# Optimization experiments

Measured on AMD Instinct MI355X. Metric: run time of the kernel, lower is better.

The kernel has to match this reference:

```python
import jax, jax.numpy as jnp
import numpy as np

DIM = 2048
NHEAD = 16
HEAD_DIM = DIM // NHEAD
FF_HIDDEN = 5632
EPS = 1e-6


def setup_inputs() -> dict:
    key = jax.random.key(0)
    ks = jax.random.split(key, 8)
    B, S = 2, 2048
    sd = 0.02
    return {
        "x": jax.random.normal(ks[0], (B, S, DIM), dtype=jnp.float32),
        "w_qkv": jax.random.normal(ks[1], (DIM, 3 * DIM), dtype=jnp.float32) * sd,
        "w_out": jax.random.normal(ks[2], (DIM, DIM), dtype=jnp.float32) * sd,
        "g1": jnp.ones((DIM,), dtype=jnp.float32),
        "g2": jnp.ones((DIM,), dtype=jnp.float32),
        "w1": jax.random.normal(ks[3], (DIM, FF_HIDDEN), dtype=jnp.float32) * sd,
        "w3": jax.random.normal(ks[4], (DIM, FF_HIDDEN), dtype=jnp.float32) * sd,
        "w2": jax.random.normal(ks[5], (FF_HIDDEN, DIM), dtype=jnp.float32) * sd,
    }


def _rmsnorm(x, g):
    rms = jnp.sqrt(jnp.mean(x * x, axis=-1, keepdims=True) + EPS)
    return x / rms * g


def _attention(x, w_qkv, w_out):
    B, S, D = x.shape
    qkv = x @ w_qkv  # [B,S,3D]
    q, k, v = jnp.split(qkv, 3, axis=-1)
    # [B,H,S,hd]
    q = q.reshape(B, S, NHEAD, HEAD_DIM).transpose(0, 2, 1, 3)
    k = k.reshape(B, S, NHEAD, HEAD_DIM).transpose(0, 2, 1, 3)
    v = v.reshape(B, S, NHEAD, HEAD_DIM).transpose(0, 2, 1, 3)
    scores = jnp.einsum("bhqd,bhkd->bhqk", q, k) / jnp.sqrt(jnp.float32(HEAD_DIM))
    causal = jnp.tril(jnp.ones((S, S), dtype=bool))
    scores = jnp.where(causal, scores, -jnp.inf)
    attn = jax.nn.softmax(scores, axis=-1)
    out = jnp.einsum("bhqk,bhkd->bhqd", attn, v)
    out = out.transpose(0, 2, 1, 3).reshape(B, S, D)
    return out @ w_out


def _swiglu(x, w1, w3, w2):
    return (jax.nn.silu(x @ w1) * (x @ w3)) @ w2


def reference(x, w_qkv, w_out, g1, g2, w1, w3, w2):
    x = x + _attention(_rmsnorm(x, g1), w_qkv, w_out)
    x = x + _swiglu(_rmsnorm(x, g2), w1, w3, w2)
    return x
```

## Files before the change

### kernel.cpp

```cpp
#include <hip/hip_runtime.h>
#include <hip/hip_bf16.h>
#include <stdint.h>


typedef __attribute__((ext_vector_type(8))) short bf16x8;
typedef __attribute__((ext_vector_type(8))) unsigned short u16x8;
typedef __attribute__((ext_vector_type(4))) float f32x4;

__device__ __forceinline__ unsigned short f2bf(float f) {
  union { float f; unsigned int u; } c; c.f = f;
  unsigned int u = c.u + 0x7fffu + ((c.u >> 16) & 1u);
  return (unsigned short)(u >> 16);
}
__device__ __forceinline__ float bf2f(unsigned short h) {
  union { unsigned int u; float f; } c; c.u = ((unsigned int)h) << 16;
  return c.f;
}

__device__ __forceinline__ void gload16(const void* g, void* l) {
  __builtin_amdgcn_global_load_lds(
      (const __attribute__((address_space(1))) void*)g,
      (__attribute__((address_space(3))) void*)l, 16, 0, 0);
}

__global__ __launch_bounds__(256)
void rmsnorm_bf16(const float* __restrict__ x, const float* __restrict__ g,
                  unsigned short* __restrict__ y)
{
  const long row = blockIdx.x;
  const float* xr = x + row * 2048;
  const int t = threadIdx.x;
  float4 a = *(const float4*)(xr + t * 8);
  float4 b = *(const float4*)(xr + t * 8 + 4);
  float ss = a.x*a.x + a.y*a.y + a.z*a.z + a.w*a.w
           + b.x*b.x + b.y*b.y + b.z*b.z + b.w*b.w;
#pragma unroll
  for (int off = 32; off >= 1; off >>= 1) ss += __shfl_xor(ss, off, 64);
  __shared__ float sm[4];
  if ((t & 63) == 0) sm[t >> 6] = ss;
  __syncthreads();
  float inv = rsqrtf((sm[0] + sm[1] + sm[2] + sm[3]) * (1.0f / 2048.0f) + 1e-6f);
  float4 ga = *(const float4*)(g + t * 8);
  float4 gb = *(const float4*)(g + t * 8 + 4);
  u16x8 ov;
  ov[0] = f2bf(a.x * inv * ga.x); ov[1] = f2bf(a.y * inv * ga.y);
  ov[2] = f2bf(a.z * inv * ga.z); ov[3] = f2bf(a.w * inv * ga.w);
  ov[4] = f2bf(b.x * inv * gb.x); ov[5] = f2bf(b.y * inv * gb.y);
  ov[6] = f2bf(b.z * inv * gb.z); ov[7] = f2bf(b.w * inv * gb.w);
  *(u16x8*)(y + row * 2048 + t * 8) = ov;
}

__global__ __launch_bounds__(256)
void transpose_w(const float* __restrict__ in, unsigned short* __restrict__ outp,
                 int K, int N)
{
  __shared__ float tile[32][33];
  const int c0 = blockIdx.x * 32, r0 = blockIdx.y * 32;
  const int cx = threadIdx.x & 31, ry = threadIdx.x >> 5;
#pragma unroll
  for (int i = 0; i < 4; i++)
    tile[ry + i * 8][cx] = in[(long)(r0 + ry + i * 8) * N + c0 + cx];
  __syncthreads();
#pragma unroll
  for (int i = 0; i < 4; i++)
    outp[(long)(c0 + ry + i * 8) * K + r0 + cx] = f2bf(tile[cx][ry + i * 8]);
}

template<int EPI>
__global__ __launch_bounds__(256)
void gemm_bt(const unsigned short* __restrict__ A,
             const unsigned short* __restrict__ Bt,
             void* __restrict__ Cout,
             const float* __restrict__ res,
             const unsigned short* __restrict__ mulsrc,
             unsigned short* __restrict__ vTout,
             int M, int N, int K)
{
  __shared__ unsigned short lds[2 * 128 * 64];
  const int tid = threadIdx.x;
  const int lane = tid & 63, wave = tid >> 6;
  const int wr = wave >> 1, wc = wave & 1;
  const int l15 = lane & 15, lg = lane >> 4;

  const int nwg = gridDim.x * gridDim.y;
  int wg = blockIdx.y * gridDim.x + blockIdx.x;
  wg = (wg & 7) * (nwg >> 3) + (wg >> 3);
  const int bx = wg % gridDim.x, by = wg / gridDim.x;
  const long m0 = (long)by * 128, n0 = (long)bx * 128;

  f32x4 acc[4][4];
#pragma unroll
  for (int m = 0; m < 4; m++)
#pragma unroll
    for (int n = 0; n < 4; n++) acc[m][n] = f32x4{0.f, 0.f, 0.f, 0.f};

  const int rsub = lane >> 3;
  const int csw = (lane & 7) ^ rsub;
  const unsigned short* Ab = A + (m0 + wave * 32 + rsub) * (long)K + csw * 8;
  const unsigned short* Bb = Bt + (n0 + wave * 32 + rsub) * (long)K + csw * 8;
  unsigned short* Al = lds + wave * 2048;
  unsigned short* Bl = lds + 8192 + wave * 2048;

  for (int kt = 0; kt < K; kt += 64) {
    __syncthreads();
#pragma unroll
    for (int i = 0; i < 4; i++) {
      gload16(Ab + (long)(i * 8) * K + kt, Al + i * 512);
      gload16(Bb + (long)(i * 8) * K + kt, Bl + i * 512);
    }
    __syncthreads();
#pragma unroll
    for (int kc = 0; kc < 2; kc++) {
      bf16x8 af[4], bfr[4];
#pragma unroll
      for (int m = 0; m < 4; m++) {
        int row = wr * 64 + m * 16 + l15;
        int off = row * 128 + ((kc * 64 + lg * 16) ^ ((row & 7) << 4));
        af[m] = *(const bf16x8*)((const char*)lds + off);
      }
#pragma unroll
      for (int n = 0; n < 4; n++) {
        int row = wc * 64 + n * 16 + l15;
        int off = 16384 + row * 128 + ((kc * 64 + lg * 16) ^ ((row & 7) << 4));
        bfr[n] = *(const bf16x8*)((const char*)lds + off);
      }
#pragma unroll
      for (int m = 0; m < 4; m++)
#pragma unroll
        for (int n = 0; n < 4; n++)
          acc[m][n] = __builtin_amdgcn_mfma_f32_16x16x32_bf16(af[m], bfr[n], acc[m][n], 0, 0, 0);
    }
  }

  if (EPI == 3) {
#pragma unroll
    for (int m = 0; m < 4; m++)
#pragma unroll
      for (int n = 0; n < 4; n++)
#pragma unroll
        for (int r = 0; r < 4; r++) {
          long row = m0 + wr * 64 + m * 16 + lg * 4 + r;
          long col = n0 + wc * 64 + n * 16 + l15;
          ((float*)Cout)[row * N + col] = acc[m][n][r] + res[row * N + col];
        }
    return;
  }

  __syncthreads();
  unsigned short* Cl = lds;
#pragma unroll
  for (int m = 0; m < 4; m++)
#pragma unroll
    for (int n = 0; n < 4; n++)
#pragma unroll
      for (int r = 0; r < 4; r++) {
        float v = acc[m][n][r];
        if (EPI == 1) v = v / (1.f + __expf(-v));
        int row = wr * 64 + m * 16 + lg * 4 + r;
        int col = wc * 64 + n * 16 + l15;
        Cl[row * 128 + (((col >> 3) ^ (row >> 3)) & 15) * 8 + (col & 7)] = f2bf(v);
      }
  __syncthreads();
#pragma unroll
  for (int r8 = 0; r8 < 8; r8++) {
    int id = tid + r8 * 256;
    int row = id >> 4, c = (id & 15) * 8;
    int ch = (id & 15) ^ (row >> 3);
    long grow = m0 + row, gcol = n0 + c;
    u16x8 v = *(const u16x8*)(Cl + row * 128 + ch * 8);
    if (EPI == 2) {
      u16x8 mm = *(const u16x8*)(mulsrc + grow * N + gcol);
#pragma unroll
      for (int j = 0; j < 8; j++) v[j] = f2bf(bf2f(v[j]) * bf2f(mm[j]));
    }
    *(u16x8*)((unsigned short*)Cout + grow * N + gcol) = v;
  }

  if (EPI == 0 && vTout != nullptr && n0 >= 4096) {
    const int hh = (int)((n0 - 4096) >> 7);
    const int b = (int)(m0 >> 11);
    const long s0 = m0 & 2047;
    unsigned short* vtb = vTout + ((long)(b * 16 + hh) * 128) * 2048;
#pragma unroll
    for (int r8 = 0; r8 < 8; r8++) {
      int id = tid + r8 * 256;
      int d = id >> 4, sc = (id & 15) * 8;
      int ch = ((d >> 3) ^ (id & 15)) & 15;
      u16x8 v;
#pragma unroll
      for (int j = 0; j < 8; j++) v[j] = Cl[(sc + j) * 128 + ch * 8 + (d & 7)];
      *(u16x8*)(vtb + (long)d * 2048 + s0 + sc) = v;
    }
  }
}

#define QSTEP(qf, mrow, lrow, o, qb, isdiag) do {                              \
    f32x4 sacc[4];                                                             \
    __builtin_amdgcn_s_setprio(1);                                             \
    _Pragma("unroll")                                                          \
    for (int cg = 0; cg < 4; cg++) {                                           \
      f32x4 a = f32x4{0.f, 0.f, 0.f, 0.f};                                     \
      _Pragma("unroll")                                                        \
      for (int kc = 0; kc < 4; kc++) {                                         \
        int krow = cg * 16 + l15;                                              \
        bf16x8 kf = *(const bf16x8*)((char*)Klds +                             \
            (krow * 256 + ((kc * 64 + lg * 16) ^ ((krow & 7) << 4))));         \
        a = __builtin_amdgcn_mfma_f32_16x16x32_bf16(qf[kc], kf, a, 0, 0, 0);   \
      }                                                                        \
      sacc[cg] = a;                                                            \
    }                                                                          \
    __builtin_amdgcn_s_setprio(0);                                             \
    float p[4][4], pm[4];                                                      \
    _Pragma("unroll")                                                          \
    for (int r = 0; r < 4; r++) pm[r] = -1e30f;                                \
    _Pragma("unroll")                                                          \
    for (int cg = 0; cg < 4; cg++)                                             \
      _Pragma("unroll")                                                        \
      for (int r = 0; r < 4; r++) {                                            \
        float v = sacc[cg][r] * scale;                                         \
        if (isdiag) {                                                          \
          int kvg = kv0 + cg * 16 + l15;                                       \
          int qg = qb + w * 16 + lg * 4 + r;                                   \
          if (kvg > qg) v = -1e30f;                                            \
        }                                                                      \
        p[cg][r] = v;                                                          \
        pm[r] = fmaxf(pm[r], v);                                               \
      }                                                                        \
    _Pragma("unroll")                                                          \
    for (int r = 0; r < 4; r++) {                                              \
      _Pragma("unroll")                                                        \
      for (int off = 1; off < 16; off <<= 1)                                   \
        pm[r] = fmaxf(pm[r], __shfl_xor(pm[r], off, 64));                      \
      float mn = fmaxf(mrow[r], pm[r]);                                        \
      float al = __expf(mrow[r] - mn);                                         \
      mrow[r] = mn;                                                            \
      float s = 0.f;                                                           \
      _Pragma("unroll")                                                        \
      for (int cg = 0; cg < 4; cg++) { p[cg][r] = __expf(p[cg][r] - mn); s += p[cg][r]; } \
      _Pragma("unroll")                                                        \
      for (int off = 1; off < 16; off <<= 1)                                   \
        s += __shfl_xor(s, off, 64);                                           \
      lrow[r] = lrow[r] * al + s;                                              \
      _Pragma("unroll")                                                        \
      for (int dg = 0; dg < 8; dg++) o[dg][r] *= al;                           \
    }                                                                          \
    _Pragma("unroll")                                                          \
    for (int cg = 0; cg < 4; cg++)                                             \
      _Pragma("unroll")                                                        \
      for (int r = 0; r < 4; r++) {                                            \
        int q = lg * 4 + r;                                                    \
        *((unsigned short*)((char*)&Plds[w][0] +                               \
            (q * 128 + (((cg * 16 + l15) * 2) ^ ((q & 7) << 4))))) = f2bf(p[cg][r]); \
      }                                                                        \
    asm volatile("s_waitcnt lgkmcnt(0)" ::: "memory");                         \
    __builtin_amdgcn_sched_barrier(0);                                         \
    __builtin_amdgcn_s_setprio(1);                                             \
    _Pragma("unroll")                                                          \
    for (int kc = 0; kc < 2; kc++) {                                           \
      bf16x8 pa = *(const bf16x8*)((char*)&Plds[w][0] +                        \
          (l15 * 128 + ((kc * 64 + lg * 16) ^ ((l15 & 7) << 4))));             \
      _Pragma("unroll")                                                        \
      for (int dg = 0; dg < 8; dg++) {                                         \
        int d = dg * 16 + l15;                                                 \
        bf16x8 vf = *(const bf16x8*)((char*)Vlds +                             \
            (d * 128 + ((kc * 64 + lg * 16) ^ ((d & 7) << 4))));               \
        o[dg] = __builtin_amdgcn_mfma_f32_16x16x32_bf16(pa, vf, o[dg], 0, 0, 0); \
      }                                                                        \
    }                                                                          \
    __builtin_amdgcn_s_setprio(0);                                             \
  } while (0)

__global__ __launch_bounds__(256, 2)
void attn_fwd(const unsigned short* __restrict__ qkv,
              const unsigned short* __restrict__ vT,
              unsigned short* __restrict__ out)
{
  __shared__ unsigned short Klds[64 * 128];
  __shared__ unsigned short Vlds[128 * 64];
  __shared__ unsigned short Plds[4][16 * 64];
  const int tid = threadIdx.x, lane = tid & 63, w = tid >> 6;
  const int l15 = lane & 15, lg = lane >> 4;

  const int nwg = gridDim.x * gridDim.y;
  int wg = blockIdx.y * gridDim.x + blockIdx.x;
  wg = (wg & 7) * (nwg >> 3) + (wg >> 3);
  const int ip = wg % 16;
  const int bh = wg / 16;
  const int b = bh >> 4, hh = bh & 15;

  const int qbA = ip * 64, qbB = (31 - ip) * 64;
  const long base = (long)b * 2048 * 6144;
  const int qoff = hh * 128, koff = 2048 + hh * 128;
  const unsigned short* vTg = vT + (long)bh * (128 * 2048);

  bf16x8 qfA[4], qfB[4];
  {
    long qrA = qbA + w * 16 + l15, qrB = qbB + w * 16 + l15;
#pragma unroll
    for (int kc = 0; kc < 4; kc++) {
      qfA[kc] = *(const bf16x8*)(qkv + base + qrA * 6144 + qoff + kc * 32 + lg * 8);
      qfB[kc] = *(const bf16x8*)(qkv + base + qrB * 6144 + qoff + kc * 32 + lg * 8);
    }
  }
  f32x4 oA[8], oB[8];
#pragma unroll
  for (int dg = 0; dg < 8; dg++) {
    oA[dg] = f32x4{0.f, 0.f, 0.f, 0.f};
    oB[dg] = f32x4{0.f, 0.f, 0.f, 0.f};
  }
  float mA[4] = {-1e30f, -1e30f, -1e30f, -1e30f}, lA[4] = {0.f, 0.f, 0.f, 0.f};
  float mB[4] = {-1e30f, -1e30f, -1e30f, -1e30f}, lB[4] = {0.f, 0.f, 0.f, 0.f};
  const float scale = 0.08838834764831845f;

  const int s_st = tid >> 4, d0 = (tid & 15) * 8;
  const int vrow = tid >> 3, vc = tid & 7;

  const int nt = 32 - ip;
  for (int t = 0; t < nt; t++) {
    const int kv0 = t * 64;
#pragma unroll
    for (int u = 0; u < 4; u++) {
      int srow = s_st + u * 16;
      uint4 kk = *(const uint4*)(qkv + base + (long)(kv0 + srow) * 6144 + koff + d0);
      *(uint4*)((char*)Klds + (srow * 256 + ((d0 * 2) ^ ((srow & 7) << 4)))) = kk;
    }
#pragma unroll
    for (int u = 0; u < 4; u++) {
      int d = vrow + u * 32;
      uint4 vv = *(const uint4*)(vTg + (long)d * 2048 + kv0 + vc * 8);
      *(uint4*)((char*)Vlds + (d * 128 + ((vc * 16) ^ ((d & 7) << 4)))) = vv;
    }
    __syncthreads();

    if (t <= ip) QSTEP(qfA, mA, lA, oA, qbA, (t == ip));
    QSTEP(qfB, mB, lB, oB, qbB, (t == nt - 1));

    __syncthreads();
  }

#pragma unroll
  for (int r = 0; r < 4; r++) {
    float invA = 1.f / lA[r], invB = 1.f / lB[r];
    long rowA = (long)b * 2048 + qbA + w * 16 + lg * 4 + r;
    long rowB = (long)b * 2048 + qbB + w * 16 + lg * 4 + r;
#pragma unroll
    for (int dg = 0; dg < 8; dg++) {
      out[rowA * 2048 + hh * 128 + dg * 16 + l15] = f2bf(oA[dg][r] * invA);
      out[rowB * 2048 + hh * 128 + dg * 16 + l15] = f2bf(oB[dg][r] * invB);
    }
  }
}

extern "C" void kernel_launch(void* const* d_in, const int* in_sizes, int n_in,
                              void* d_out, int out_size, void* d_ws, size_t ws_size,
                              hipStream_t stream)
{
  const float* x     = (const float*)d_in[0];
  const float* w_qkv = (const float*)d_in[1];
  const float* w_out = (const float*)d_in[2];
  const float* g1    = (const float*)d_in[3];
  const float* g2    = (const float*)d_in[4];
  const float* w1    = (const float*)d_in[5];
  const float* w3    = (const float*)d_in[6];
  const float* w2    = (const float*)d_in[7];
  float* outp = (float*)d_out;
  char* ws = (char*)d_ws;

  unsigned short* wT  = (unsigned short*)(ws);
  unsigned short* y   = (unsigned short*)(ws + 25165824);
  unsigned short* qkv = (unsigned short*)(ws + 41943040);
  unsigned short* att = (unsigned short*)(ws + 92274688);
  float*          x1  = (float*)(ws + 109051904);
  unsigned short* s1  = (unsigned short*)(ws + 142606336);
  unsigned short* vTb = s1;
  unsigned short* h   = qkv;

  rmsnorm_bf16<<<4096, 256, 0, stream>>>(x, g1, y);
  transpose_w<<<dim3(192, 64), 256, 0, stream>>>(w_qkv, wT, 2048, 6144);
  gemm_bt<0><<<dim3(48, 32), 256, 0, stream>>>(y, wT, qkv, nullptr, nullptr, vTb, 4096, 6144, 2048);
  attn_fwd<<<dim3(16, 32), 256, 0, stream>>>(qkv, vTb, att);
  transpose_w<<<dim3(64, 64), 256, 0, stream>>>(w_out, wT, 2048, 2048);
  gemm_bt<3><<<dim3(16, 32), 256, 0, stream>>>(att, wT, x1, x, nullptr, nullptr, 4096, 2048, 2048);

  rmsnorm_bf16<<<4096, 256, 0, stream>>>(x1, g2, y);
  transpose_w<<<dim3(176, 64), 256, 0, stream>>>(w1, wT, 2048, 5632);
  gemm_bt<1><<<dim3(44, 32), 256, 0, stream>>>(y, wT, s1, nullptr, nullptr, nullptr, 4096, 5632, 2048);
  transpose_w<<<dim3(176, 64), 256, 0, stream>>>(w3, wT, 2048, 5632);
  gemm_bt<2><<<dim3(44, 32), 256, 0, stream>>>(y, wT, h, nullptr, s1, nullptr, 4096, 5632, 2048);
  transpose_w<<<dim3(64, 176), 256, 0, stream>>>(w2, wT, 5632, 2048);
  gemm_bt<3><<<dim3(16, 32), 256, 0, stream>>>(h, wT, outp, x1, nullptr, nullptr, 4096, 2048, 5632);
}
```

Baseline: 711.0 us.

## Use 64-row GEMM tiles for N=2048 projections and store residual in bf16

Adds a gemm_mt64 kernel with 64x128 tiles for the two N=2048 GEMMs (out-projection and down-projection). This doubles the workgroup count from 512 to 1024 so more CUs have work. The intermediate residual x1 is now stored in bf16 rather than fp32, and a new bf16-input rmsnorm reads it. The final GEMM adds the bf16 residual back. The new kernel has a simpler single-buffered K loop, and the bf16 residual loses precision in the skip connection.

```diff
diff --git a/kernel.cpp b/kernel.cpp
--- a/kernel.cpp
+++ b/kernel.cpp
@@ -51,6 +51,34 @@
 }
 
 __global__ __launch_bounds__(256)
+void rmsnorm_bf16_in(const unsigned short* __restrict__ x, const float* __restrict__ g,
+                     unsigned short* __restrict__ y)
+{
+  const long row = blockIdx.x;
+  const unsigned short* xr = x + row * 2048;
+  const int t = threadIdx.x;
+  u16x8 iv = *(const u16x8*)(xr + t * 8);
+  float v[8];
+  float ss = 0.f;
+#pragma unroll
+  for (int j = 0; j < 8; j++) { v[j] = bf2f(iv[j]); ss += v[j] * v[j]; }
+#pragma unroll
+  for (int off = 32; off >= 1; off >>= 1) ss += __shfl_xor(ss, off, 64);
+  __shared__ float sm[4];
+  if ((t & 63) == 0) sm[t >> 6] = ss;
+  __syncthreads();
+  float inv = rsqrtf((sm[0] + sm[1] + sm[2] + sm[3]) * (1.0f / 2048.0f) + 1e-6f);
+  float4 ga = *(const float4*)(g + t * 8);
+  float4 gb = *(const float4*)(g + t * 8 + 4);
+  u16x8 ov;
+  ov[0] = f2bf(v[0] * inv * ga.x); ov[1] = f2bf(v[1] * inv * ga.y);
+  ov[2] = f2bf(v[2] * inv * ga.z); ov[3] = f2bf(v[3] * inv * ga.w);
+  ov[4] = f2bf(v[4] * inv * gb.x); ov[5] = f2bf(v[5] * inv * gb.y);
+  ov[6] = f2bf(v[6] * inv * gb.z); ov[7] = f2bf(v[7] * inv * gb.w);
+  *(u16x8*)(y + row * 2048 + t * 8) = ov;
+}
+
+__global__ __launch_bounds__(256)
 void transpose_w(const float* __restrict__ in, unsigned short* __restrict__ outp,
                  int K, int N)
 {
@@ -191,6 +219,110 @@
       for (int j = 0; j < 8; j++) v[j] = Cl[(sc + j) * 128 + ch * 8 + (d & 7)];
       *(u16x8*)(vtb + (long)d * 2048 + s0 + sc) = v;
     }
+  }
+}
+
+template<int EPI>
+__global__ __launch_bounds__(256)
+void gemm_mt64(const unsigned short* __restrict__ A,
+               const unsigned short* __restrict__ Bt,
+               void* __restrict__ Cout,
+               const float* __restrict__ res,
+               const unsigned short* __restrict__ res16,
+               int M, int N, int K)
+{
+  __shared__ unsigned short lds[64 * 64 + 128 * 64];
+  const int tid = threadIdx.x;
+  const int lane = tid & 63, wave = tid >> 6;
+  const int wr = wave >> 1, wc = wave & 1;
+  const int l15 = lane & 15, lg = lane >> 4;
+
+  const int nwg = gridDim.x * gridDim.y;
+  int wg = blockIdx.y * gridDim.x + blockIdx.x;
+  wg = (wg & 7) * (nwg >> 3) + (wg >> 3);
+  const int bx = wg % gridDim.x, by = wg / gridDim.x;
+  const long m0 = (long)by * 64, n0 = (long)bx * 128;
+
+  f32x4 acc[2][4];
+#pragma unroll
+  for (int m = 0; m < 2; m++)
+#pragma unroll
+    for (int n = 0; n < 4; n++) acc[m][n] = f32x4{0.f, 0.f, 0.f, 0.f};
+
+  const int rsub = lane >> 3;
+  const int csw = (lane & 7) ^ rsub;
+  const unsigned short* Ab = A + (m0 + wave * 16 + rsub) * (long)K + csw * 8;
+  const unsigned short* Bb = Bt + (n0 + wave * 32 + rsub) * (long)K + csw * 8;
+  unsigned short* Al = lds + wave * 1024;
+  unsigned short* Bl = lds + 4096 + wave * 2048;
+
+  for (int kt = 0; kt < K; kt += 64) {
+    __syncthreads();
+#pragma unroll
+    for (int i = 0; i < 2; i++)
+      gload16(Ab + (long)(i * 8) * K + kt, Al + i * 512);
+#pragma unroll
+    for (int i = 0; i < 4; i++)
+      gload16(Bb + (long)(i * 8) * K + kt, Bl + i * 512);
+    __syncthreads();
+#pragma unroll
+    for (int kc = 0; kc < 2; kc++) {
+      bf16x8 af[2], bfr[4];
+#pragma unroll
+      for (int m = 0; m < 2; m++) {
+        int row = wr * 32 + m * 16 + l15;
+        int off = row * 128 + ((kc * 64 + lg * 16) ^ ((row & 7) << 4));
+        af[m] = *(const bf16x8*)((const char*)lds + off);
+      }
+#pragma unroll
+      for (int n = 0; n < 4; n++) {
+        int row = wc * 64 + n * 16 + l15;
+        int off = 8192 + row * 128 + ((kc * 64 + lg * 16) ^ ((row & 7) << 4));
+        bfr[n] = *(const bf16x8*)((const char*)lds + off);
+      }
+#pragma unroll
+      for (int m = 0; m < 2; m++)
+#pragma unroll
+        for (int n = 0; n < 4; n++)
+          acc[m][n] = __builtin_amdgcn_mfma_f32_16x16x32_bf16(af[m], bfr[n], acc[m][n], 0, 0, 0);
+    }
+  }
+
+  if (EPI == 5) {
+#pragma unroll
+    for (int m = 0; m < 2; m++)
+#pragma unroll
+      for (int n = 0; n < 4; n++)
+#pragma unroll
+        for (int r = 0; r < 4; r++) {
+          long row = m0 + wr * 32 + m * 16 + lg * 4 + r;
+          long col = n0 + wc * 64 + n * 16 + l15;
+          ((float*)Cout)[row * N + col] = acc[m][n][r] + bf2f(res16[row * N + col]);
+        }
+    return;
+  }
+
+  __syncthreads();
+  unsigned short* Cl = lds;
+#pragma unroll
+  for (int m = 0; m < 2; m++)
+#pragma unroll
+    for (int n = 0; n < 4; n++)
+#pragma unroll
+      for (int r = 0; r < 4; r++) {
+        int row = wr * 32 + m * 16 + lg * 4 + r;
+        int col = wc * 64 + n * 16 + l15;
+        float v = acc[m][n][r] + res[(m0 + row) * N + n0 + col];
+        Cl[row * 128 + (((col >> 3) ^ (row >> 3)) & 15) * 8 + (col & 7)] = f2bf(v);
+      }
+  __syncthreads();
+#pragma unroll
+  for (int rnd = 0; rnd < 4; rnd++) {
+    int id = tid + rnd * 256;
+    int row = id >> 4, c = (id & 15) * 8;
+    int ch = (id & 15) ^ (row >> 3);
+    u16x8 v = *(const u16x8*)(Cl + row * 128 + ch * 8);
+    *(u16x8*)((unsigned short*)Cout + (m0 + row) * N + n0 + c) = v;
   }
 }
 
@@ -370,7 +502,7 @@
   unsigned short* y   = (unsigned short*)(ws + 25165824);
   unsigned short* qkv = (unsigned short*)(ws + 41943040);
   unsigned short* att = (unsigned short*)(ws + 92274688);
-  float*          x1  = (float*)(ws + 109051904);
+  unsigned short* x1b = (unsigned short*)(ws + 109051904);
   unsigned short* s1  = (unsigned short*)(ws + 142606336);
   unsigned short* vTb = s1;
   unsigned short* h   = qkv;
@@ -380,13 +512,13 @@
   gemm_bt<0><<<dim3(48, 32), 256, 0, stream>>>(y, wT, qkv, nullptr, nullptr, vTb, 4096, 6144, 2048);
   attn_fwd<<<dim3(16, 32), 256, 0, stream>>>(qkv, vTb, att);
   transpose_w<<<dim3(64, 64), 256, 0, stream>>>(w_out, wT, 2048, 2048);
-  gemm_bt<3><<<dim3(16, 32), 256, 0, stream>>>(att, wT, x1, x, nullptr, nullptr, 4096, 2048, 2048);
-
-  rmsnorm_bf16<<<4096, 256, 0, stream>>>(x1, g2, y);
+  gemm_mt64<4><<<dim3(16, 64), 256, 0, stream>>>(att, wT, x1b, x, nullptr, 4096, 2048, 2048);
+
+  rmsnorm_bf16_in<<<4096, 256, 0, stream>>>(x1b, g2, y);
   transpose_w<<<dim3(176, 64), 256, 0, stream>>>(w1, wT, 2048, 5632);
   gemm_bt<1><<<dim3(44, 32), 256, 0, stream>>>(y, wT, s1, nullptr, nullptr, nullptr, 4096, 5632, 2048);
   transpose_w<<<dim3(176, 64), 256, 0, stream>>>(w3, wT, 2048, 5632);
   gemm_bt<2><<<dim3(44, 32), 256, 0, stream>>>(y, wT, h, nullptr, s1, nullptr, 4096, 5632, 2048);
   transpose_w<<<dim3(64, 176), 256, 0, stream>>>(w2, wT, 5632, 2048);
-  gemm_bt<3><<<dim3(16, 32), 256, 0, stream>>>(h, wT, outp, x1, nullptr, nullptr, 4096, 2048, 5632);
-}
+  gemm_mt64<5><<<dim3(16, 64), 256, 0, stream>>>(h, wT, outp, nullptr, x1b, 4096, 2048, 5632);
+}
```

Result: no change. 710.5 us (-0.1%).
